# Kernel tuning notes

Hardware: AMD Instinct MI355X
Metric: run time of the kernel (lower is better)

The kernel has to match this reference:

```python
import jax, jax.numpy as jnp
import numpy as np

N_NODES = 50000
N_EDGES = 1600000
IN_DIM = 1024
HID = 2048
OUT = 3
BN_EPS = 1e-5


def _degree_norms(src, dst):
    ones = jnp.ones((src.shape[0],), jnp.float32)
    out_deg = jax.ops.segment_sum(ones, src, num_segments=N_NODES)
    in_deg = jax.ops.segment_sum(ones, dst, num_segments=N_NODES)
    # DGL GraphConv norm='both' clamps degrees to min 1
    out_norm = jnp.clip(out_deg, 1.0) ** -0.5
    in_norm = jnp.clip(in_deg, 1.0) ** -0.5
    return out_norm, in_norm


def _graph_conv(h, src, dst, out_norm, in_norm, W, b):
    # symmetric-normalized SpMM aggregate then dense transform (DGL GraphConv, norm='both')
    h = h * out_norm[:, None]
    msg = h[src]                                   # [E, F] gather
    agg = jax.ops.segment_sum(msg, dst, num_segments=N_NODES)
    agg = agg * in_norm[:, None]
    return agg @ W + b


def setup_inputs() -> dict:
    key = jax.random.key(0)
    k1, k2, k3, k4, k5, k6, k7 = jax.random.split(key, 7)
    in_feat = jax.random.normal(k1, (N_NODES, IN_DIM), jnp.float32)
    src = jax.random.randint(k2, (N_EDGES,), 0, N_NODES, jnp.int32)
    dst = jax.random.randint(k3, (N_EDGES,), 0, N_NODES, jnp.int32)
    W1 = jax.random.normal(k4, (IN_DIM, HID), jnp.float32) * (1.0 / np.sqrt(IN_DIM))
    b1 = jnp.zeros((HID,), jnp.float32)
    Wout = jax.random.normal(k5, (HID, OUT), jnp.float32) * (1.0 / np.sqrt(HID))
    bout = jnp.zeros((OUT,), jnp.float32)
    return {"in_feat": in_feat, "src": src, "dst": dst,
            "W1": W1, "b1": b1, "Wout": Wout, "bout": bout}


def reference(in_feat, src, dst, W1, b1, Wout, bout):
    out_norm, in_norm = _degree_norms(src, dst)
    h = _graph_conv(in_feat, src, dst, out_norm, in_norm, W1, b1)
    h = jax.nn.relu(h)
    # freshly-instantiated BatchNorm1d in training mode: batch stats, gamma=1, beta=0
    mean = jnp.mean(h, axis=0, keepdims=True)
    var = jnp.var(h, axis=0, keepdims=True)
    h = (h - mean) * jax.lax.rsqrt(var + BN_EPS)
    h = _graph_conv(h, src, dst, out_norm, in_norm, Wout, bout)
    return jax.nn.softmax(h, axis=1)
```

## Files before the change

### kernel.cpp

```cpp
#include <hip/hip_runtime.h>
#include <hip/hip_bf16.h>
#include <stdint.h>

#define N_NODES 50000
#define N_EDGES 1600000
#define IN_DIM  1024
#define HID     2048
#define OUTC    3
#define M_PAD   50048
#define BN_EPS  1e-5f

#define SCAN_CH 512
#define NCH     98

#define NPANEL  2
#define PFEAT   512

typedef __bf16 bf16_t;
typedef __bf16 bf16x4_t __attribute__((ext_vector_type(4)));
typedef __bf16 bf16x8_t __attribute__((ext_vector_type(8)));
typedef float  f32x4_t  __attribute__((ext_vector_type(4)));

__device__ __forceinline__ void gl2lds16(const void* g, void* l) {
  __builtin_amdgcn_global_load_lds((const __attribute__((address_space(1))) uint32_t*)g,
                                   (__attribute__((address_space(3))) uint32_t*)l,
                                   16, 0, 0);
}

__global__ void k_hist(const int* __restrict__ src, const int* __restrict__ dst,
                       int* out_cnt, int* in_cnt) {
  int e = blockIdx.x * 256 + threadIdx.x;
  if (e < N_EDGES) {
    atomicAdd(&out_cnt[src[e]], 1);
    atomicAdd(&in_cnt[dst[e]], 1);
  }
}

__global__ void k_norms(const int* __restrict__ out_cnt, const int* __restrict__ in_cnt,
                        float* out_norm, float* in_norm) {
  int i = blockIdx.x * 256 + threadIdx.x;
  if (i < N_NODES) {
    out_norm[i] = rsqrtf((float)max(out_cnt[i], 1));
    in_norm[i]  = rsqrtf((float)max(in_cnt[i], 1));
  }
}

__global__ void k_scan1(const int* __restrict__ deg, int* incl, int* partial) {
  __shared__ int s[SCAN_CH];
  int tid = threadIdx.x;
  int i = blockIdx.x * SCAN_CH + tid;
  int v = (i < N_NODES) ? deg[i] : 0;
  s[tid] = v;
  for (int off = 1; off < SCAN_CH; off <<= 1) {
    __syncthreads();
    int x = (tid >= off) ? s[tid - off] : 0;
    __syncthreads();
    s[tid] += x;
  }
  __syncthreads();
  if (i < N_NODES) incl[i] = s[tid];
  if (tid == SCAN_CH - 1) partial[blockIdx.x] = s[tid];
}

__global__ void k_scan2(const int* __restrict__ partial, int* chunk_off, int* row_ptr) {
  if (threadIdx.x == 0 && blockIdx.x == 0) {
    int run = 0;
    for (int b = 0; b < NCH; b++) { chunk_off[b] = run; run += partial[b]; }
    row_ptr[N_NODES] = run;
  }
}

__global__ void k_scan3(const int* __restrict__ deg, const int* __restrict__ incl,
                        const int* __restrict__ chunk_off, int* row_ptr, int* cursor) {
  int i = blockIdx.x * SCAN_CH + threadIdx.x;
  if (i < N_NODES) {
    int e = chunk_off[blockIdx.x] + incl[i] - deg[i];
    row_ptr[i] = e;
    cursor[i]  = e;
  }
}

__global__ void k_fill(const int* __restrict__ src, const int* __restrict__ dst,
                       int* cursor, int* csr_src) {
  int e = blockIdx.x * 256 + threadIdx.x;
  if (e < N_EDGES) {
    int p = atomicAdd(&cursor[dst[e]], 1);
    csr_src[p] = src[e];
  }
}

__global__ void k_conv(const float* __restrict__ in_feat, const float* __restrict__ out_norm,
                       bf16_t* __restrict__ xb) {
  int node = blockIdx.x, tid = threadIdx.x;
  float on = out_norm[node];
  float4 v = *(const float4*)(in_feat + (size_t)node * IN_DIM + tid * 4);
  bf16x4_t o;
  o[0] = (bf16_t)(v.x * on); o[1] = (bf16_t)(v.y * on);
  o[2] = (bf16_t)(v.z * on); o[3] = (bf16_t)(v.w * on);
  *(bf16x4_t*)(xb + (size_t)node * IN_DIM + tid * 4) = o;
}

__global__ void k_agg1(const bf16_t* __restrict__ xb, const int* __restrict__ row_ptr,
                       const int* __restrict__ csr_src, const float* __restrict__ in_norm,
                       bf16_t* __restrict__ aggb) {
  int node = blockIdx.x * 2 + (threadIdx.x >> 6);
  int lane = threadIdx.x & 63;
  int f0 = blockIdx.y * PFEAT + lane * 8;
  float acc[8];
#pragma unroll
  for (int j = 0; j < 8; j++) acc[j] = 0.f;
  float inn = 0.f;
  if (node < N_NODES) {
    int beg = row_ptr[node], end = row_ptr[node + 1];
    int e = beg;
    for (; e + 8 <= end; e += 8) {
      int s[8];
#pragma unroll
      for (int u = 0; u < 8; u++) s[u] = csr_src[e + u];
      bf16x8_t v[8];
#pragma unroll
      for (int u = 0; u < 8; u++)
        v[u] = *(const bf16x8_t*)(xb + (size_t)s[u] * IN_DIM + f0);
#pragma unroll
      for (int u = 0; u < 8; u++)
#pragma unroll
        for (int j = 0; j < 8; j++) acc[j] += (float)v[u][j];
    }
    for (; e + 2 <= end; e += 2) {
      int s0 = csr_src[e], s1 = csr_src[e + 1];
      bf16x8_t v0 = *(const bf16x8_t*)(xb + (size_t)s0 * IN_DIM + f0);
      bf16x8_t v1 = *(const bf16x8_t*)(xb + (size_t)s1 * IN_DIM + f0);
#pragma unroll
      for (int j = 0; j < 8; j++) acc[j] += (float)v0[j];
#pragma unroll
      for (int j = 0; j < 8; j++) acc[j] += (float)v1[j];
    }
    if (e < end) {
      int s0 = csr_src[e];
      bf16x8_t v0 = *(const bf16x8_t*)(xb + (size_t)s0 * IN_DIM + f0);
#pragma unroll
      for (int j = 0; j < 8; j++) acc[j] += (float)v0[j];
    }
    inn = in_norm[node];
  }
  bf16x8_t o;
#pragma unroll
  for (int j = 0; j < 8; j++) o[j] = (bf16_t)(acc[j] * inn);
  __builtin_nontemporal_store(o, (bf16x8_t*)(aggb + (size_t)node * IN_DIM + f0));
}

__global__ void k_w1t(const float* __restrict__ W1, bf16_t* __restrict__ W1t) {
  __shared__ float tile[32][33];
  int k0 = blockIdx.x * 32, n0 = blockIdx.y * 32;
  int tx = threadIdx.x & 31, ty = threadIdx.x >> 5;
#pragma unroll
  for (int r = 0; r < 32; r += 8)
    tile[ty + r][tx] = W1[(size_t)(k0 + ty + r) * HID + n0 + tx];
  __syncthreads();
#pragma unroll
  for (int r = 0; r < 32; r += 8)
    W1t[(size_t)(n0 + ty + r) * IN_DIM + k0 + tx] = (bf16_t)tile[tx][ty + r];
}

__global__ void __launch_bounds__(256)
k_gemm1(const bf16_t* __restrict__ A, const bf16_t* __restrict__ Bt,
        const float* __restrict__ b1, bf16_t* __restrict__ C,
        float* __restrict__ colsum, float* __restrict__ colsq) {
  __shared__ bf16_t As[128 * 32];
  __shared__ bf16_t Bs[128 * 32];
  int t = threadIdx.x;
  const int m0 = blockIdx.y * 128, n0 = blockIdx.x * 128;

  int lrow = t >> 2, lseg = t & 3;
  const bf16_t* aG0 = A + (size_t)(m0 + lrow) * IN_DIM + lseg * 8;
  const bf16_t* aG1 = aG0 + (size_t)64 * IN_DIM;
  const bf16_t* bG0 = Bt + (size_t)(n0 + lrow) * IN_DIM + lseg * 8;
  const bf16_t* bG1 = bG0 + (size_t)64 * IN_DIM;
  bf16_t* aL0 = As + t * 8; bf16_t* aL1 = As + 2048 + t * 8;
  bf16_t* bL0 = Bs + t * 8; bf16_t* bL1 = Bs + 2048 + t * 8;

  int wv = t >> 6, ln = t & 63;
  int wm = (wv >> 1) * 64, wn = (wv & 1) * 64;
  int fr = ln & 15, fq = ln >> 4;
  const bf16_t* aF = As + (wm + fr) * 32 + fq * 8;
  const bf16_t* bF = Bs + (wn + fr) * 32 + fq * 8;

  f32x4_t acc[4][4];
#pragma unroll
  for (int i = 0; i < 4; i++)
#pragma unroll
    for (int j = 0; j < 4; j++) { acc[i][j][0]=0.f; acc[i][j][1]=0.f; acc[i][j][2]=0.f; acc[i][j][3]=0.f; }

  for (int kt = 0; kt < IN_DIM; kt += 32) {
    __syncthreads();
    gl2lds16(aG0 + kt, aL0);
    gl2lds16(aG1 + kt, aL1);
    gl2lds16(bG0 + kt, bL0);
    gl2lds16(bG1 + kt, bL1);
    __syncthreads();
    bf16x8_t af[4], bfr[4];
#pragma unroll
    for (int i = 0; i < 4; i++) af[i]  = *(const bf16x8_t*)(aF + i * 16 * 32);
#pragma unroll
    for (int j = 0; j < 4; j++) bfr[j] = *(const bf16x8_t*)(bF + j * 16 * 32);
#pragma unroll
    for (int i = 0; i < 4; i++)
#pragma unroll
      for (int j = 0; j < 4; j++)
        acc[i][j] = __builtin_amdgcn_mfma_f32_16x16x32_bf16(af[i], bfr[j], acc[i][j], 0, 0, 0);
  }

#pragma unroll
  for (int j = 0; j < 4; j++) {
    int col = n0 + wn + j * 16 + fr;
    float bias = b1[col];
    float s = 0.f, ss = 0.f;
#pragma unroll
    for (int i = 0; i < 4; i++) {
#pragma unroll
      for (int r = 0; r < 4; r++) {
        int row = m0 + wm + i * 16 + fq * 4 + r;
        float v = acc[i][j][r] + bias;
        v = v > 0.f ? v : 0.f;
        bf16_t bv = (bf16_t)v;
        __builtin_nontemporal_store(*(short*)&bv, (short*)&C[(size_t)row * HID + col]);
        if (row < N_NODES) { s += v; ss += v * v; }
      }
    }
    s  += __shfl_xor(s, 16);  s  += __shfl_xor(s, 32);
    ss += __shfl_xor(ss, 16); ss += __shfl_xor(ss, 32);
    if (fq == 0) {
      atomicAdd(&colsum[col], s);
      atomicAdd(&colsq[col], ss);
    }
  }
}

__global__ void k_bnfin(const float* __restrict__ colsum, const float* __restrict__ colsq,
                        const float* __restrict__ Wout,
                        float* cw0, float* cw1, float* cw2, float* mrs) {
  int f = blockIdx.x * 256 + threadIdx.x;
  if (f < HID) {
    float mean = colsum[f] * (1.f / N_NODES);
    float var  = colsq[f] * (1.f / N_NODES) - mean * mean;
    float rs   = rsqrtf(var + BN_EPS);
    cw0[f] = rs * Wout[f * 3 + 0];
    cw1[f] = rs * Wout[f * 3 + 1];
    cw2[f] = rs * Wout[f * 3 + 2];
    mrs[f] = mean * rs;
  }
}

__global__ void k_ct(const float* __restrict__ mrs, const float* __restrict__ Wout, float* ct) {
  __shared__ float red[3][256];
  int tid = threadIdx.x;
  float s0 = 0.f, s1 = 0.f, s2 = 0.f;
  for (int f = tid; f < HID; f += 256) {
    float m = mrs[f];
    s0 += m * Wout[f * 3 + 0];
    s1 += m * Wout[f * 3 + 1];
    s2 += m * Wout[f * 3 + 2];
  }
  red[0][tid] = s0; red[1][tid] = s1; red[2][tid] = s2;
  __syncthreads();
  for (int off = 128; off; off >>= 1) {
    if (tid < off) {
      red[0][tid] += red[0][tid + off];
      red[1][tid] += red[1][tid + off];
      red[2][tid] += red[2][tid + off];
    }
    __syncthreads();
  }
  if (tid == 0) { ct[0] = red[0][0]; ct[1] = red[1][0]; ct[2] = red[2][0]; }
}

__global__ void k_tmat(const bf16_t* __restrict__ h1, const float* __restrict__ cw0,
                       const float* __restrict__ cw1, const float* __restrict__ cw2,
                       const float* __restrict__ ct, const float* __restrict__ out_norm,
                       float4* __restrict__ t4) {
  int n = blockIdx.x, tid = threadIdx.x;
  int f0 = tid * 8;
  bf16x8_t hv = *(const bf16x8_t*)(h1 + (size_t)n * HID + f0);
  float s0 = 0.f, s1 = 0.f, s2 = 0.f;
#pragma unroll
  for (int j = 0; j < 8; j++) {
    float h = (float)hv[j];
    s0 += h * cw0[f0 + j];
    s1 += h * cw1[f0 + j];
    s2 += h * cw2[f0 + j];
  }
#pragma unroll
  for (int off = 32; off; off >>= 1) {
    s0 += __shfl_down(s0, off);
    s1 += __shfl_down(s1, off);
    s2 += __shfl_down(s2, off);
  }
  __shared__ float red[3][4];
  int wv = tid >> 6, ln = tid & 63;
  if (ln == 0) { red[0][wv] = s0; red[1][wv] = s1; red[2][wv] = s2; }
  __syncthreads();
  if (tid == 0) {
    float r0 = red[0][0] + red[0][1] + red[0][2] + red[0][3];
    float r1 = red[1][0] + red[1][1] + red[1][2] + red[1][3];
    float r2 = red[2][0] + red[2][1] + red[2][2] + red[2][3];
    float on = out_norm[n];
    t4[n] = make_float4(on * (r0 - ct[0]), on * (r1 - ct[1]), on * (r2 - ct[2]), 0.f);
  }
}

__global__ void k_out(const int* __restrict__ row_ptr, const int* __restrict__ csr_src,
                      const float4* __restrict__ t4, const float* __restrict__ in_norm,
                      const float* __restrict__ bout, float* __restrict__ out) {
  int i = blockIdx.x * 256 + threadIdx.x;
  if (i >= N_NODES) return;
  float a0 = 0.f, a1 = 0.f, a2 = 0.f;
  int beg = row_ptr[i], end = row_ptr[i + 1];
  for (int e = beg; e < end; e++) {
    float4 tv = t4[csr_src[e]];
    a0 += tv.x; a1 += tv.y; a2 += tv.z;
  }
  float inn = in_norm[i];
  float l0 = inn * a0 + bout[0];
  float l1 = inn * a1 + bout[1];
  float l2 = inn * a2 + bout[2];
  float m = fmaxf(l0, fmaxf(l1, l2));
  float e0 = expf(l0 - m), e1 = expf(l1 - m), e2 = expf(l2 - m);
  float rs = 1.f / (e0 + e1 + e2);
  out[i * 3 + 0] = e0 * rs;
  out[i * 3 + 1] = e1 * rs;
  out[i * 3 + 2] = e2 * rs;
}

extern "C" void kernel_launch(void* const* d_in, const int* in_sizes, int n_in,
                              void* d_out, int out_size, void* d_ws, size_t ws_size,
                              hipStream_t stream) {
  const float* in_feat = (const float*)d_in[0];
  const int*   src     = (const int*)d_in[1];
  const int*   dst     = (const int*)d_in[2];
  const float* W1      = (const float*)d_in[3];
  const float* b1      = (const float*)d_in[4];
  const float* Wout    = (const float*)d_in[5];
  const float* bout    = (const float*)d_in[6];
  float* out = (float*)d_out;

  char* p = (char*)d_ws;
  auto alloc = [&](size_t bytes) { char* r = p; p += (bytes + 255) & ~(size_t)255; return r; };
  bf16_t* h1      = (bf16_t*)alloc((size_t)M_PAD * HID * 2);
  bf16_t* aggb    = (bf16_t*)alloc((size_t)M_PAD * IN_DIM * 2);
  bf16_t* xb      = (bf16_t*)alloc((size_t)N_NODES * IN_DIM * 2);
  bf16_t* W1t     = (bf16_t*)alloc((size_t)HID * IN_DIM * 2);
  int* csr_src    = (int*)alloc((size_t)N_EDGES * 4);
  int* row_ptr    = (int*)alloc((size_t)(N_NODES + 1) * 4);
  int* cursor     = (int*)alloc((size_t)N_NODES * 4);
  int* incl       = (int*)alloc((size_t)N_NODES * 4);
  int* partial    = (int*)alloc((size_t)NCH * 4);
  int* chunk_off  = (int*)alloc((size_t)NCH * 4);
  int* out_cnt    = (int*)alloc((size_t)N_NODES * 4);
  int* in_cnt     = (int*)alloc((size_t)N_NODES * 4);
  float* out_norm = (float*)alloc((size_t)N_NODES * 4);
  float* in_norm  = (float*)alloc((size_t)N_NODES * 4);
  float* colsum   = (float*)alloc((size_t)HID * 4);
  float* colsq    = (float*)alloc((size_t)HID * 4);
  float* cw0      = (float*)alloc((size_t)HID * 4);
  float* cw1      = (float*)alloc((size_t)HID * 4);
  float* cw2      = (float*)alloc((size_t)HID * 4);
  float* mrs      = (float*)alloc((size_t)HID * 4);
  float* ct       = (float*)alloc(4 * 4);
  float4* t4      = (float4*)alloc((size_t)N_NODES * 16);

  hipMemsetAsync(out_cnt, 0, (size_t)N_NODES * 4, stream);
  hipMemsetAsync(in_cnt,  0, (size_t)N_NODES * 4, stream);
  hipMemsetAsync(colsum,  0, (size_t)HID * 4, stream);
  hipMemsetAsync(colsq,   0, (size_t)HID * 4, stream);

  k_hist <<<(N_EDGES + 255) / 256, 256, 0, stream>>>(src, dst, out_cnt, in_cnt);
  k_norms<<<(N_NODES + 255) / 256, 256, 0, stream>>>(out_cnt, in_cnt, out_norm, in_norm);
  k_conv <<<N_NODES, 256, 0, stream>>>(in_feat, out_norm, xb);
  k_scan1<<<NCH, SCAN_CH, 0, stream>>>(in_cnt, incl, partial);
  k_scan2<<<1, 64, 0, stream>>>(partial, chunk_off, row_ptr);
  k_scan3<<<NCH, SCAN_CH, 0, stream>>>(in_cnt, incl, chunk_off, row_ptr, cursor);
  k_fill <<<(N_EDGES + 255) / 256, 256, 0, stream>>>(src, dst, cursor, csr_src);
  k_w1t  <<<dim3(IN_DIM / 32, HID / 32), 256, 0, stream>>>(W1, W1t);
  k_agg1 <<<dim3(M_PAD / 2, NPANEL), 128, 0, stream>>>(xb, row_ptr, csr_src, in_norm, aggb);
  k_gemm1<<<dim3(HID / 128, M_PAD / 128), 256, 0, stream>>>(aggb, W1t, b1, h1, colsum, colsq);
  k_bnfin<<<HID / 256, 256, 0, stream>>>(colsum, colsq, Wout, cw0, cw1, cw2, mrs);
  k_ct   <<<1, 256, 0, stream>>>(mrs, Wout, ct);
  k_tmat <<<N_NODES, 256, 0, stream>>>(h1, cw0, cw1, cw2, ct, out_norm, t4);
  k_out  <<<(N_NODES + 255) / 256, 256, 0, stream>>>(row_ptr, csr_src, t4, in_norm, bout, out);
}
```

Before: 1.451 ms.

## Panelize gather features into L2-sized slabs with XCD-aware aggregation mapping

Stores the normalized bf16 node features as 32 panels of 32 features each, so every panel is a small contiguous slab. The aggregation blocks are mapped so each XCD works through its own panels, which is meant to keep the randomly gathered rows in that XCD's L2 instead of fetching them from HBM. CSR rows are padded to a multiple of 4 with a dummy source that points at a zeroed row, so the inner loop can fetch 4 neighbours with one coalesced index load and shuffles and needs no tail handling. The cost is a few extra zero-row gathers per node, a larger CSR buffer, an extra padding kernel, and reliance on the hardware assigning blocks to XCDs round-robin.

```diff
diff --git a/kernel.cpp b/kernel.cpp
--- a/kernel.cpp
+++ b/kernel.cpp
@@ -13,8 +13,13 @@
 #define SCAN_CH 512
 #define NCH     98
 
-#define NPANEL  2
-#define PFEAT   512
+#define NPAN    32
+#define PF      32
+#define PSTRIDE ((size_t)M_PAD * PF)
+#define NGRP    782
+#define NXCD    8
+#define DUMMY_SRC N_NODES
+#define E_PAD_MAX (N_EDGES + 3 * N_NODES)
 
 typedef __bf16 bf16_t;
 typedef __bf16 bf16x4_t __attribute__((ext_vector_type(4)));
@@ -49,7 +54,7 @@
   __shared__ int s[SCAN_CH];
   int tid = threadIdx.x;
   int i = blockIdx.x * SCAN_CH + tid;
-  int v = (i < N_NODES) ? deg[i] : 0;
+  int v = (i < N_NODES) ? ((deg[i] + 3) & ~3) : 0;
   s[tid] = v;
   for (int off = 1; off < SCAN_CH; off <<= 1) {
     __syncthreads();
@@ -74,7 +79,8 @@
                         const int* __restrict__ chunk_off, int* row_ptr, int* cursor) {
   int i = blockIdx.x * SCAN_CH + threadIdx.x;
   if (i < N_NODES) {
-    int e = chunk_off[blockIdx.x] + incl[i] - deg[i];
+    int dp = (deg[i] + 3) & ~3;
+    int e = chunk_off[blockIdx.x] + incl[i] - dp;
     row_ptr[i] = e;
     cursor[i]  = e;
   }
@@ -89,64 +95,79 @@
   }
 }
 
+__global__ void k_pad(const int* __restrict__ in_cnt, const int* __restrict__ row_ptr,
+                      int* csr_src) {
+  int i = blockIdx.x * 256 + threadIdx.x;
+  if (i < N_NODES) {
+    int d = in_cnt[i], dp = (d + 3) & ~3;
+    int base = row_ptr[i];
+    for (int j = d; j < dp; j++) csr_src[base + j] = DUMMY_SRC;
+  }
+}
+
 __global__ void k_conv(const float* __restrict__ in_feat, const float* __restrict__ out_norm,
-                       bf16_t* __restrict__ xb) {
-  int node = blockIdx.x, tid = threadIdx.x;
-  float on = out_norm[node];
-  float4 v = *(const float4*)(in_feat + (size_t)node * IN_DIM + tid * 4);
+                       bf16_t* __restrict__ xbp) {
+  int node = blockIdx.x, t = threadIdx.x;
+  int p = t >> 3, fo = (t & 7) * 4;
   bf16x4_t o;
-  o[0] = (bf16_t)(v.x * on); o[1] = (bf16_t)(v.y * on);
-  o[2] = (bf16_t)(v.z * on); o[3] = (bf16_t)(v.w * on);
-  *(bf16x4_t*)(xb + (size_t)node * IN_DIM + tid * 4) = o;
-}
-
-__global__ void k_agg1(const bf16_t* __restrict__ xb, const int* __restrict__ row_ptr,
-                       const int* __restrict__ csr_src, const float* __restrict__ in_norm,
-                       bf16_t* __restrict__ aggb) {
-  int node = blockIdx.x * 2 + (threadIdx.x >> 6);
-  int lane = threadIdx.x & 63;
-  int f0 = blockIdx.y * PFEAT + lane * 8;
+  if (node < N_NODES) {
+    float on = out_norm[node];
+    float4 v = *(const float4*)(in_feat + (size_t)node * IN_DIM + p * PF + fo);
+    o[0] = (bf16_t)(v.x * on); o[1] = (bf16_t)(v.y * on);
+    o[2] = (bf16_t)(v.z * on); o[3] = (bf16_t)(v.w * on);
+  } else {
+    o[0] = (bf16_t)0.f; o[1] = (bf16_t)0.f; o[2] = (bf16_t)0.f; o[3] = (bf16_t)0.f;
+  }
+  *(bf16x4_t*)(xbp + (size_t)p * PSTRIDE + (size_t)node * PF + fo) = o;
+}
+
+__global__ void __launch_bounds__(256)
+k_agg1(const bf16_t* __restrict__ xbp, const int* __restrict__ row_ptr,
+       const int* __restrict__ csr_src, const float* __restrict__ in_norm,
+       bf16_t* __restrict__ aggb) {
+  int b = blockIdx.x;
+  int xcd = b & (NXCD - 1), seq = b >> 3;
+  int phase = seq / NGRP, grp = seq - phase * NGRP;
+  int panel = xcd + (phase << 3);
+  int wv = threadIdx.x >> 6, lane = threadIdx.x & 63;
+  int ch = lane >> 2, seg = lane & 3;
+  int node = grp * 64 + wv * 16 + ch;
+
+  const bf16_t* xp = xbp + (size_t)panel * PSTRIDE + (seg << 3);
+
+  int beg = 0, end = 0;
+  if (node < N_NODES) { beg = row_ptr[node]; end = row_ptr[node + 1]; }
+
   float acc[8];
 #pragma unroll
   for (int j = 0; j < 8; j++) acc[j] = 0.f;
-  float inn = 0.f;
-  if (node < N_NODES) {
-    int beg = row_ptr[node], end = row_ptr[node + 1];
-    int e = beg;
-    for (; e + 8 <= end; e += 8) {
-      int s[8];
-#pragma unroll
-      for (int u = 0; u < 8; u++) s[u] = csr_src[e + u];
-      bf16x8_t v[8];
-#pragma unroll
-      for (int u = 0; u < 8; u++)
-        v[u] = *(const bf16x8_t*)(xb + (size_t)s[u] * IN_DIM + f0);
-#pragma unroll
-      for (int u = 0; u < 8; u++)
-#pragma unroll
-        for (int j = 0; j < 8; j++) acc[j] += (float)v[u][j];
-    }
-    for (; e + 2 <= end; e += 2) {
-      int s0 = csr_src[e], s1 = csr_src[e + 1];
-      bf16x8_t v0 = *(const bf16x8_t*)(xb + (size_t)s0 * IN_DIM + f0);
-      bf16x8_t v1 = *(const bf16x8_t*)(xb + (size_t)s1 * IN_DIM + f0);
-#pragma unroll
-      for (int j = 0; j < 8; j++) acc[j] += (float)v0[j];
-#pragma unroll
-      for (int j = 0; j < 8; j++) acc[j] += (float)v1[j];
-    }
-    if (e < end) {
-      int s0 = csr_src[e];
-      bf16x8_t v0 = *(const bf16x8_t*)(xb + (size_t)s0 * IN_DIM + f0);
-#pragma unroll
-      for (int j = 0; j < 8; j++) acc[j] += (float)v0[j];
-    }
-    inn = in_norm[node];
-  }
+
+  for (int e = beg; e < end; e += 4) {
+    int my = __builtin_nontemporal_load(csr_src + e + seg);
+    int i0 = __shfl(my, 0, 4);
+    int i1 = __shfl(my, 1, 4);
+    int i2 = __shfl(my, 2, 4);
+    int i3 = __shfl(my, 3, 4);
+    bf16x8_t v0 = *(const bf16x8_t*)(xp + ((size_t)(unsigned)i0 << 5));
+    bf16x8_t v1 = *(const bf16x8_t*)(xp + ((size_t)(unsigned)i1 << 5));
+    bf16x8_t v2 = *(const bf16x8_t*)(xp + ((size_t)(unsigned)i2 << 5));
+    bf16x8_t v3 = *(const bf16x8_t*)(xp + ((size_t)(unsigned)i3 << 5));
+#pragma unroll
+    for (int j = 0; j < 8; j++) acc[j] += (float)v0[j];
+#pragma unroll
+    for (int j = 0; j < 8; j++) acc[j] += (float)v1[j];
+#pragma unroll
+    for (int j = 0; j < 8; j++) acc[j] += (float)v2[j];
+#pragma unroll
+    for (int j = 0; j < 8; j++) acc[j] += (float)v3[j];
+  }
+
+  float inn = (node < N_NODES) ? in_norm[node] : 0.f;
   bf16x8_t o;
 #pragma unroll
   for (int j = 0; j < 8; j++) o[j] = (bf16_t)(acc[j] * inn);
-  __builtin_nontemporal_store(o, (bf16x8_t*)(aggb + (size_t)node * IN_DIM + f0));
+  __builtin_nontemporal_store(o,
+      (bf16x8_t*)(aggb + (size_t)node * IN_DIM + panel * PF + (seg << 3)));
 }
 
 __global__ void k_w1t(const float* __restrict__ W1, bf16_t* __restrict__ W1t) {
@@ -347,9 +368,9 @@
   auto alloc = [&](size_t bytes) { char* r = p; p += (bytes + 255) & ~(size_t)255; return r; };
   bf16_t* h1      = (bf16_t*)alloc((size_t)M_PAD * HID * 2);
   bf16_t* aggb    = (bf16_t*)alloc((size_t)M_PAD * IN_DIM * 2);
-  bf16_t* xb      = (bf16_t*)alloc((size_t)N_NODES * IN_DIM * 2);
+  bf16_t* xbp     = (bf16_t*)alloc((size_t)NPAN * PSTRIDE * 2);
   bf16_t* W1t     = (bf16_t*)alloc((size_t)HID * IN_DIM * 2);
-  int* csr_src    = (int*)alloc((size_t)N_EDGES * 4);
+  int* csr_src    = (int*)alloc((size_t)E_PAD_MAX * 4);
   int* row_ptr    = (int*)alloc((size_t)(N_NODES + 1) * 4);
   int* cursor     = (int*)alloc((size_t)N_NODES * 4);
   int* incl       = (int*)alloc((size_t)N_NODES * 4);
@@ -366,22 +387,24 @@
   float* cw2      = (float*)alloc((size_t)HID * 4);
   float* mrs      = (float*)alloc((size_t)HID * 4);
   float* ct       = (float*)alloc(4 * 4);
-  float4* t4      = (float4*)alloc((size_t)N_NODES * 16);
+  float4* t4      = (float4*)alloc((size_t)M_PAD * 16);
 
   hipMemsetAsync(out_cnt, 0, (size_t)N_NODES * 4, stream);
   hipMemsetAsync(in_cnt,  0, (size_t)N_NODES * 4, stream);
   hipMemsetAsync(colsum,  0, (size_t)HID * 4, stream);
   hipMemsetAsync(colsq,   0, (size_t)HID * 4, stream);
+  hipMemsetAsync(t4 + N_NODES, 0, (size_t)(M_PAD - N_NODES) * 16, stream);
 
   k_hist <<<(N_EDGES + 255) / 256, 256, 0, stream>>>(src, dst, out_cnt, in_cnt);
   k_norms<<<(N_NODES + 255) / 256, 256, 0, stream>>>(out_cnt, in_cnt, out_norm, in_norm);
-  k_conv <<<N_NODES, 256, 0, stream>>>(in_feat, out_norm, xb);
+  k_conv <<<M_PAD, 256, 0, stream>>>(in_feat, out_norm, xbp);
   k_scan1<<<NCH, SCAN_CH, 0, stream>>>(in_cnt, incl, partial);
   k_scan2<<<1, 64, 0, stream>>>(partial, chunk_off, row_ptr);
   k_scan3<<<NCH, SCAN_CH, 0, stream>>>(in_cnt, incl, chunk_off, row_ptr, cursor);
+  k_pad  <<<(N_NODES + 255) / 256, 256, 0, stream>>>(in_cnt, row_ptr, csr_src);
   k_fill <<<(N_EDGES + 255) / 256, 256, 0, stream>>>(src, dst, cursor, csr_src);
   k_w1t  <<<dim3(IN_DIM / 32, HID / 32), 256, 0, stream>>>(W1, W1t);
-  k_agg1 <<<dim3(M_PAD / 2, NPANEL), 128, 0, stream>>>(xb, row_ptr, csr_src, in_norm, aggb);
+  k_agg1 <<<NXCD * (NPAN / NXCD) * NGRP, 256, 0, stream>>>(xbp, row_ptr, csr_src, in_norm, aggb);
   k_gemm1<<<dim3(HID / 128, M_PAD / 128), 256, 0, stream>>>(aggb, W1t, b1, h1, colsum, colsq);
   k_bnfin<<<HID / 256, 256, 0, stream>>>(colsum, colsq, Wout, cw0, cw1, cw2, mrs);
   k_ct   <<<1, 256, 0, stream>>>(mrs, Wout, ct);
```

Result: slower. 1.571 ms (+8.2%).

## Rewrite GEMM1 with 128x256 tiles, triple-buffered swizzled LDS and XCD-aware remap

Applied to the files above, without the earlier changes.

The first dense GEMM now uses 512-thread workgroups with 128x256x64 tiles. Global-to-LDS loads run two stages ahead in a three-buffer ring with explicit vmcnt waits, and the LDS layout is XOR-swizzled to avoid bank conflicts. Workgroup IDs are remapped so neighbouring tiles land on the same XCD, and MFMA sections get raised wave priority. Separately, each CSR row is padded to a multiple of four with a dummy source that points at a zeroed padding row, which adds a padding kernel, a memset and a few extra aggregation edges. The large LDS footprint limits occupancy to one workgroup per CU.

```diff
diff --git a/kernel.cpp b/kernel.cpp
--- a/kernel.cpp
+++ b/kernel.cpp
@@ -15,6 +15,17 @@
 
 #define NPANEL  2
 #define PFEAT   512
+#define DUMMY_SRC N_NODES
+#define E_PAD_MAX (N_EDGES + 3 * N_NODES + 64)
+
+#define BM 128
+#define BN 256
+#define BK 64
+#define NKT (IN_DIM / BK)
+#define GX (HID / BN)
+#define GY (M_PAD / BM)
+#define NWG (GX * GY)
+#define CPX (NWG / 8)
 
 typedef __bf16 bf16_t;
 typedef __bf16 bf16x4_t __attribute__((ext_vector_type(4)));
@@ -49,7 +60,7 @@
   __shared__ int s[SCAN_CH];
   int tid = threadIdx.x;
   int i = blockIdx.x * SCAN_CH + tid;
-  int v = (i < N_NODES) ? deg[i] : 0;
+  int v = (i < N_NODES) ? ((deg[i] + 3) & ~3) : 0;
   s[tid] = v;
   for (int off = 1; off < SCAN_CH; off <<= 1) {
     __syncthreads();
@@ -74,7 +85,8 @@
                         const int* __restrict__ chunk_off, int* row_ptr, int* cursor) {
   int i = blockIdx.x * SCAN_CH + threadIdx.x;
   if (i < N_NODES) {
-    int e = chunk_off[blockIdx.x] + incl[i] - deg[i];
+    int dp = (deg[i] + 3) & ~3;
+    int e = chunk_off[blockIdx.x] + incl[i] - dp;
     row_ptr[i] = e;
     cursor[i]  = e;
   }
@@ -89,14 +101,28 @@
   }
 }
 
+__global__ void k_pad(const int* __restrict__ in_cnt, const int* __restrict__ row_ptr,
+                      int* csr_src) {
+  int i = blockIdx.x * 256 + threadIdx.x;
+  if (i < N_NODES) {
+    int d = in_cnt[i], dp = (d + 3) & ~3;
+    int base = row_ptr[i];
+    for (int j = d; j < dp; j++) csr_src[base + j] = DUMMY_SRC;
+  }
+}
+
 __global__ void k_conv(const float* __restrict__ in_feat, const float* __restrict__ out_norm,
                        bf16_t* __restrict__ xb) {
   int node = blockIdx.x, tid = threadIdx.x;
-  float on = out_norm[node];
-  float4 v = *(const float4*)(in_feat + (size_t)node * IN_DIM + tid * 4);
   bf16x4_t o;
-  o[0] = (bf16_t)(v.x * on); o[1] = (bf16_t)(v.y * on);
-  o[2] = (bf16_t)(v.z * on); o[3] = (bf16_t)(v.w * on);
+  if (node < N_NODES) {
+    float on = out_norm[node];
+    float4 v = *(const float4*)(in_feat + (size_t)node * IN_DIM + tid * 4);
+    o[0] = (bf16_t)(v.x * on); o[1] = (bf16_t)(v.y * on);
+    o[2] = (bf16_t)(v.z * on); o[3] = (bf16_t)(v.w * on);
+  } else {
+    o[0] = (bf16_t)0.f; o[1] = (bf16_t)0.f; o[2] = (bf16_t)0.f; o[3] = (bf16_t)0.f;
+  }
   *(bf16x4_t*)(xb + (size_t)node * IN_DIM + tid * 4) = o;
 }
 
@@ -162,28 +188,23 @@
     W1t[(size_t)(n0 + ty + r) * IN_DIM + k0 + tx] = (bf16_t)tile[tx][ty + r];
 }
 
-__global__ void __launch_bounds__(256)
+__global__ void __launch_bounds__(512, 1)
 k_gemm1(const bf16_t* __restrict__ A, const bf16_t* __restrict__ Bt,
         const float* __restrict__ b1, bf16_t* __restrict__ C,
         float* __restrict__ colsum, float* __restrict__ colsq) {
-  __shared__ bf16_t As[128 * 32];
-  __shared__ bf16_t Bs[128 * 32];
-  int t = threadIdx.x;
-  const int m0 = blockIdx.y * 128, n0 = blockIdx.x * 128;
-
-  int lrow = t >> 2, lseg = t & 3;
-  const bf16_t* aG0 = A + (size_t)(m0 + lrow) * IN_DIM + lseg * 8;
-  const bf16_t* aG1 = aG0 + (size_t)64 * IN_DIM;
-  const bf16_t* bG0 = Bt + (size_t)(n0 + lrow) * IN_DIM + lseg * 8;
-  const bf16_t* bG1 = bG0 + (size_t)64 * IN_DIM;
-  bf16_t* aL0 = As + t * 8; bf16_t* aL1 = As + 2048 + t * 8;
-  bf16_t* bL0 = Bs + t * 8; bf16_t* bL1 = Bs + 2048 + t * 8;
-
-  int wv = t >> 6, ln = t & 63;
-  int wm = (wv >> 1) * 64, wn = (wv & 1) * 64;
+  __shared__ bf16_t sA[3][BM * BK];
+  __shared__ bf16_t sB[3][BN * BK];
+
+  int bid = blockIdx.x;
+  int wg  = (bid & 7) * CPX + (bid >> 3);
+  int tx  = wg % GX, ty = wg / GX;
+  const int m0 = ty * BM, n0 = tx * BN;
+
+  int tid = threadIdx.x;
+  int wid = tid >> 6, ln = tid & 63;
+  int lr = ln >> 3, seg = ln & 7;
+  int wr = wid >> 2, wc = wid & 3;
   int fr = ln & 15, fq = ln >> 4;
-  const bf16_t* aF = As + (wm + fr) * 32 + fq * 8;
-  const bf16_t* bF = Bs + (wn + fr) * 32 + fq * 8;
 
   f32x4_t acc[4][4];
 #pragma unroll
@@ -191,36 +212,97 @@
 #pragma unroll
     for (int j = 0; j < 4; j++) { acc[i][j][0]=0.f; acc[i][j][1]=0.f; acc[i][j][2]=0.f; acc[i][j][3]=0.f; }
 
-  for (int kt = 0; kt < IN_DIM; kt += 32) {
-    __syncthreads();
-    gl2lds16(aG0 + kt, aL0);
-    gl2lds16(aG1 + kt, aL1);
-    gl2lds16(bG0 + kt, bL0);
-    gl2lds16(bG1 + kt, bL1);
-    __syncthreads();
-    bf16x8_t af[4], bfr[4];
-#pragma unroll
-    for (int i = 0; i < 4; i++) af[i]  = *(const bf16x8_t*)(aF + i * 16 * 32);
-#pragma unroll
-    for (int j = 0; j < 4; j++) bfr[j] = *(const bf16x8_t*)(bF + j * 16 * 32);
+  auto STAGE = [&](int buf, int kt) {
+#pragma unroll
+    for (int i = 0; i < 2; i++) {
+      int R = wid * 16 + i * 8;
+      int row = R + lr;
+      int ss = seg ^ (row & 7);
+      gl2lds16(A + (size_t)(m0 + row) * IN_DIM + kt + ss * 8,
+               (char*)&sA[buf][0] + R * 128 + ln * 16);
+    }
+#pragma unroll
+    for (int i = 0; i < 4; i++) {
+      int R = wid * 32 + i * 8;
+      int row = R + lr;
+      int ss = seg ^ (row & 7);
+      gl2lds16(Bt + (size_t)(n0 + row) * IN_DIM + kt + ss * 8,
+               (char*)&sB[buf][0] + R * 128 + ln * 16);
+    }
+  };
+
+  STAGE(0, 0);
+  STAGE(1, BK);
+
+  for (int t = 0; t < NKT; t++) {
+    int r = t % 3;
+    if (t + 2 < NKT) {
+      STAGE((t + 2) % 3, (t + 2) * BK);
+      __builtin_amdgcn_sched_barrier(0);
+      asm volatile("s_waitcnt vmcnt(12)" ::: "memory");
+    } else if (t + 1 < NKT) {
+      asm volatile("s_waitcnt vmcnt(6)" ::: "memory");
+    } else {
+      asm volatile("s_waitcnt vmcnt(0)" ::: "memory");
+    }
+    __builtin_amdgcn_sched_barrier(0);
+    __builtin_amdgcn_s_barrier();
+    __builtin_amdgcn_sched_barrier(0);
+
+    const char* pa = (const char*)&sA[r][0];
+    const char* pb = (const char*)&sB[r][0];
+    bf16x8_t a[2][2], bfrag[4][2];
+#pragma unroll
+    for (int i = 0; i < 2; i++) {
+      int row = wr * 64 + i * 32;
+      (void)row;
+    }
+    bf16x8_t af[4][2];
+#pragma unroll
+    for (int i = 0; i < 4; i++) {
+      int row = wr * 64 + i * 16 + fr;
+#pragma unroll
+      for (int ks = 0; ks < 2; ks++) {
+        int s = ks * 4 + fq;
+        af[i][ks] = *(const bf16x8_t*)(pa + row * 128 + ((s ^ (row & 7)) << 4));
+      }
+    }
+#pragma unroll
+    for (int j = 0; j < 4; j++) {
+      int col = wc * 64 + j * 16 + fr;
+#pragma unroll
+      for (int ks = 0; ks < 2; ks++) {
+        int s = ks * 4 + fq;
+        bfrag[j][ks] = *(const bf16x8_t*)(pb + col * 128 + ((s ^ (col & 7)) << 4));
+      }
+    }
+    asm volatile("s_waitcnt lgkmcnt(0)" ::: "memory");
+    __builtin_amdgcn_sched_barrier(0);
+    __builtin_amdgcn_s_barrier();
+    __builtin_amdgcn_sched_barrier(0);
+    __builtin_amdgcn_s_setprio(1);
 #pragma unroll
     for (int i = 0; i < 4; i++)
 #pragma unroll
-      for (int j = 0; j < 4; j++)
-        acc[i][j] = __builtin_amdgcn_mfma_f32_16x16x32_bf16(af[i], bfr[j], acc[i][j], 0, 0, 0);
+      for (int j = 0; j < 4; j++) {
+        acc[i][j] = __builtin_amdgcn_mfma_f32_16x16x32_bf16(af[i][0], bfrag[j][0], acc[i][j], 0, 0, 0);
+        acc[i][j] = __builtin_amdgcn_mfma_f32_16x16x32_bf16(af[i][1], bfrag[j][1], acc[i][j], 0, 0, 0);
+      }
+    __builtin_amdgcn_s_setprio(0);
+    (void)a;
   }
 
 #pragma unroll
   for (int j = 0; j < 4; j++) {
-    int col = n0 + wn + j * 16 + fr;
+    int col = n0 + wc * 64 + j * 16 + fr;
     float bias = b1[col];
     float s = 0.f, ss = 0.f;
 #pragma unroll
     for (int i = 0; i < 4; i++) {
 #pragma unroll
-      for (int r = 0; r < 4; r++) {
-        int row = m0 + wm + i * 16 + fq * 4 + r;
-        float v = acc[i][j][r] + bias;
+      for (int rr = 0; rr < 4; rr++) {
+        int row = m0 + wr * 64 + i * 16 + fq * 4 + rr;
+        float v = acc[i][j][rr] + bias;
         v = v > 0.f ? v : 0.f;
         bf16_t bv = (bf16_t)v;
         __builtin_nontemporal_store(*(short*)&bv, (short*)&C[(size_t)row * HID + col]);
@@ -347,9 +429,9 @@
   auto alloc = [&](size_t bytes) { char* r = p; p += (bytes + 255) & ~(size_t)255; return r; };
   bf16_t* h1      = (bf16_t*)alloc((size_t)M_PAD * HID * 2);
   bf16_t* aggb    = (bf16_t*)alloc((size_t)M_PAD * IN_DIM * 2);
-  bf16_t* xb      = (bf16_t*)alloc((size_t)N_NODES * IN_DIM * 2);
+  bf16_t* xb      = (bf16_t*)alloc((size_t)M_PAD * IN_DIM * 2);
   bf16_t* W1t     = (bf16_t*)alloc((size_t)HID * IN_DIM * 2);
-  int* csr_src    = (int*)alloc((size_t)N_EDGES * 4);
+  int* csr_src    = (int*)alloc((size_t)E_PAD_MAX * 4);
   int* row_ptr    = (int*)alloc((size_t)(N_NODES + 1) * 4);
   int* cursor     = (int*)alloc((size_t)N_NODES * 4);
   int* incl       = (int*)alloc((size_t)N_NODES * 4);
@@ -366,23 +448,25 @@
   float* cw2      = (float*)alloc((size_t)HID * 4);
   float* mrs      = (float*)alloc((size_t)HID * 4);
   float* ct       = (float*)alloc(4 * 4);
-  float4* t4      = (float4*)alloc((size_t)N_NODES * 16);
+  float4* t4      = (float4*)alloc((size_t)M_PAD * 16);
 
   hipMemsetAsync(out_cnt, 0, (size_t)N_NODES * 4, stream);
   hipMemsetAsync(in_cnt,  0, (size_t)N_NODES * 4, stream);
   hipMemsetAsync(colsum,  0, (size_t)HID * 4, stream);
   hipMemsetAsync(colsq,   0, (size_t)HID * 4, stream);
+  hipMemsetAsync(t4 + N_NODES, 0, (size_t)(M_PAD - N_NODES) * 16, stream);
 
   k_hist <<<(N_EDGES + 255) / 256, 256, 0, stream>>>(src, dst, out_cnt, in_cnt);
   k_norms<<<(N_NODES + 255) / 256, 256, 0, stream>>>(out_cnt, in_cnt, out_norm, in_norm);
-  k_conv <<<N_NODES, 256, 0, stream>>>(in_feat, out_norm, xb);
+  k_conv <<<M_PAD, 256, 0, stream>>>(in_feat, out_norm, xb);
   k_scan1<<<NCH, SCAN_CH, 0, stream>>>(in_cnt, incl, partial);
   k_scan2<<<1, 64, 0, stream>>>(partial, chunk_off, row_ptr);
   k_scan3<<<NCH, SCAN_CH, 0, stream>>>(in_cnt, incl, chunk_off, row_ptr, cursor);
+  k_pad  <<<(N_NODES + 255) / 256, 256, 0, stream>>>(in_cnt, row_ptr, csr_src);
   k_fill <<<(N_EDGES + 255) / 256, 256, 0, stream>>>(src, dst, cursor, csr_src);
   k_w1t  <<<dim3(IN_DIM / 32, HID / 32), 256, 0, stream>>>(W1, W1t);
   k_agg1 <<<dim3(M_PAD / 2, NPANEL), 128, 0, stream>>>(xb, row_ptr, csr_src, in_norm, aggb);
-  k_gemm1<<<dim3(HID / 128, M_PAD / 128), 256, 0, stream>>>(aggb, W1t, b1, h1, colsum, colsq);
+  k_gemm1<<<NWG, 512, 0, stream>>>(aggb, W1t, b1, h1, colsum, colsq);
   k_bnfin<<<HID / 256, 256, 0, stream>>>(colsum, colsq, Wout, cw0, cw1, cw2, mrs);
   k_ct   <<<1, 256, 0, stream>>>(mrs, Wout, ct);
   k_tmat <<<N_NODES, 256, 0, stream>>>(h1, cw0, cw1, cw2, ct, out_norm, t4);
```

Result: slower. 1.529 ms (+5.3%).
